# Kernel optimization log

Hardware: AMD Instinct MI355X
Metric: run time of the kernel (lower is better)

The kernel has to match this reference:

```python
import jax, jax.numpy as jnp
import numpy as np

HIDDEN = 768
HEADS = 12
HEAD_DIM = HIDDEN // HEADS


def setup_inputs() -> dict:
    key = jax.random.key(0)
    ks = jax.random.split(key, 9)
    B, S = 2, 2048
    scale = 1.0 / np.sqrt(HIDDEN)
    return {
        "hidden_states": jax.random.normal(ks[0], (B, S, HIDDEN), jnp.float32),
        "context": jax.random.normal(ks[1], (B, S, HIDDEN), jnp.float32),
        "attention_mask": jnp.zeros((B, 1, 1, S), jnp.float32),
        "Wq": jax.random.normal(ks[2], (HIDDEN, HIDDEN), jnp.float32) * scale,
        "bq": jnp.zeros((HIDDEN,), jnp.float32),
        "Wk": jax.random.normal(ks[3], (HIDDEN, HIDDEN), jnp.float32) * scale,
        "bk": jnp.zeros((HIDDEN,), jnp.float32),
        "Wv": jax.random.normal(ks[4], (HIDDEN, HIDDEN), jnp.float32) * scale,
        "bv": jnp.zeros((HIDDEN,), jnp.float32),
    }


def _split_heads(x):
    # [B, S, H*D] -> [B, H, S, D]
    B, S, _ = x.shape
    return x.reshape(B, S, HEADS, HEAD_DIM).transpose(0, 2, 1, 3)


def reference(hidden_states, context, attention_mask, Wq, bq, Wk, bk, Wv, bv):
    # torch Linear: y = x @ W^T + b
    q = _split_heads(hidden_states @ Wq.T + bq)   # [B,H,Sq,D]
    k = _split_heads(context @ Wk.T + bk)         # [B,H,Sk,D]
    v = _split_heads(context @ Wv.T + bv)         # [B,H,Sk,D]

    scores = jnp.einsum("bhqd,bhkd->bhqk", q, k)
    scores = scores / np.sqrt(HEAD_DIM + 1e-05)
    scores = scores + attention_mask
    probs = jax.nn.softmax(scores, axis=-1)       # dropout p=0 -> identity (eval)
    ctx = jnp.einsum("bhqk,bhkd->bhqd", probs, v) # [B,H,Sq,D]
    B, H, Sq, D = ctx.shape
    return ctx.transpose(0, 2, 1, 3).reshape(B, Sq, H * D)
```

## Files before the change

kernel.cpp:

```cpp
#include <hip/hip_runtime.h>
#include <hip/hip_bf16.h>
#include <math.h>

typedef short s16x8 __attribute__((ext_vector_type(8)));
typedef float f32x4 __attribute__((ext_vector_type(4)));
typedef _Float16 f16x4 __attribute__((ext_vector_type(4)));
typedef __fp16 fp16x2 __attribute__((ext_vector_type(2)));
typedef unsigned short u16;

#define NHEADS 12
#define SEQ 2048
#define NBH 24
#define KDIM 768
#define NSPL 4
#define LOG2E 1.44269504088896f

#define SWZ(row, col) (((row) * 64) + ((col) ^ (((row) & 7) << 3)))

#define GLOAD_LDS16(g, l) __builtin_amdgcn_global_load_lds( \
    (const __attribute__((address_space(1))) unsigned int*)(g), \
    (__attribute__((address_space(3))) unsigned int*)(l), 16, 0, 0)

static __device__ __forceinline__ u16 f2bf(float f) {
    union { float f; unsigned u; } v; v.f = f;
    unsigned r = v.u + 0x7fffu + ((v.u >> 16) & 1u);
    return (u16)(r >> 16);
}
static __device__ __forceinline__ u16 f2h(float f) {
    union { _Float16 h; u16 u; } v; v.h = (_Float16)f;
    return v.u;
}
static __device__ __forceinline__ f16x4 pack4(float a, float b, float c, float d) {
    union { fp16x2 h2[2]; f16x4 h4; } u;
    u.h2[0] = __builtin_amdgcn_cvt_pkrtz(a, b);
    u.h2[1] = __builtin_amdgcn_cvt_pkrtz(c, d);
    return u.h4;
}

__global__ void cvt6_kernel(const float* __restrict__ s0, const float* __restrict__ s1,
                            const float* __restrict__ s2, const float* __restrict__ s3,
                            const float* __restrict__ s4, const float* __restrict__ s5,
                            u16* __restrict__ d0, u16* __restrict__ d1, u16* __restrict__ d2,
                            u16* __restrict__ d3, u16* __restrict__ d4, float* __restrict__ d5,
                            int n4a, int n4w, float qscl) {
    const int z = blockIdx.z;
    int i = blockIdx.x * blockDim.x + threadIdx.x;
    if (z == 5) {
        if (i < (2 * SEQ) / 4) {
            float4 f = ((const float4*)s5)[i];
            f.x *= LOG2E; f.y *= LOG2E; f.z *= LOG2E; f.w *= LOG2E;
            ((float4*)d5)[i] = f;
        }
        return;
    }
    const float* src = (z == 0) ? s0 : (z == 1) ? s1 : (z == 2) ? s2 : (z == 3) ? s3 : s4;
    u16* dst         = (z == 0) ? d0 : (z == 1) ? d1 : (z == 2) ? d2 : (z == 3) ? d3 : d4;
    const int n4     = (z < 2) ? n4a : n4w;
    const float scl  = (z == 2) ? qscl : 1.0f;
    if (i < n4) {
        float4 f = ((const float4*)src)[i];
        ushort4 o;
        o.x = f2bf(f.x * scl); o.y = f2bf(f.y * scl); o.z = f2bf(f.z * scl); o.w = f2bf(f.w * scl);
        ((ushort4*)dst)[i] = o;
    }
}

__launch_bounds__(256)
__global__ void qkv_gemm(const u16* __restrict__ X, const u16* __restrict__ C,
                         const u16* __restrict__ W0, const u16* __restrict__ W1, const u16* __restrict__ W2,
                         const float* __restrict__ b0, const float* __restrict__ b1, const float* __restrict__ b2,
                         u16* __restrict__ Qo, u16* __restrict__ Ko, u16* __restrict__ Vo, float qscl) {
    const int z = blockIdx.z;
    const u16* A    = (z == 0) ? X  : C;
    const u16* W    = (z == 0) ? W0 : (z == 1) ? W1 : W2;
    const float* bi = (z == 0) ? b0 : (z == 1) ? b1 : b2;
    u16* out        = (z == 0) ? Qo : (z == 1) ? Ko : Vo;
    const float bscl = (z == 0) ? qscl : 1.0f;

    __shared__ u16 As[3][4096];
    __shared__ u16 Bs[3][4096];

    const int tid  = threadIdx.x;
    const int lane = tid & 63;
    const int wid  = tid >> 6;
    const int wr = wid >> 1, wc = wid & 1;
    const int l15 = lane & 15, lh = lane >> 4;
    const int mBase = blockIdx.x * 128;
    const int nBase = blockIdx.y * 128;

    size_t aSrc[2], bSrc[2]; int ldsOff[2];
    #pragma unroll
    for (int i = 0; i < 2; ++i) {
        int L = i * 2048 + tid * 8;
        int prow = L >> 6;
        int pcol = (L & 63) ^ ((prow & 7) << 3);
        int row = (prow << 1) | (pcol >> 5);
        int col = pcol & 31;
        aSrc[i] = (size_t)(mBase + row) * KDIM + col;
        bSrc[i] = (size_t)(nBase + row) * KDIM + col;
        ldsOff[i] = i * 2048 + wid * 512;
    }

#define G_STAGE(step, buf) do { \
        const size_t kb_ = (size_t)(step) * 32; \
        GLOAD_LDS16(&A[aSrc[0] + kb_], &As[buf][ldsOff[0]]); \
        GLOAD_LDS16(&A[aSrc[1] + kb_], &As[buf][ldsOff[1]]); \
        GLOAD_LDS16(&W[bSrc[0] + kb_], &Bs[buf][ldsOff[0]]); \
        GLOAD_LDS16(&W[bSrc[1] + kb_], &Bs[buf][ldsOff[1]]); \
    } while (0)

    f32x4 acc[4][4] = {};

    G_STAGE(0, 0);
    G_STAGE(1, 1);

    const int NIT = KDIM / 32;
    int cur = 0;
    for (int it = 0; it < NIT; ++it) {
        if (it + 1 < NIT) asm volatile("s_waitcnt vmcnt(4)" ::: "memory");
        else              asm volatile("s_waitcnt vmcnt(0)" ::: "memory");
        __builtin_amdgcn_s_barrier();
        __builtin_amdgcn_sched_barrier(0);

        s16x8 xf[4], wf[4];
        #pragma unroll
        for (int m = 0; m < 4; ++m) {
            int row = wr * 64 + m * 16 + l15;
            xf[m] = *(const s16x8*)(&As[cur][SWZ(row >> 1, (row & 1) * 32 + lh * 8)]);
        }
        #pragma unroll
        for (int n = 0; n < 4; ++n) {
            int row = wc * 64 + n * 16 + l15;
            wf[n] = *(const s16x8*)(&Bs[cur][SWZ(row >> 1, (row & 1) * 32 + lh * 8)]);
        }
        if (z < 2) {
            #pragma unroll
            for (int m = 0; m < 4; ++m)
                #pragma unroll
                for (int n = 0; n < 4; ++n)
                    acc[m][n] = __builtin_amdgcn_mfma_f32_16x16x32_bf16(wf[n], xf[m], acc[m][n], 0, 0, 0);
        } else {
            #pragma unroll
            for (int m = 0; m < 4; ++m)
                #pragma unroll
                for (int n = 0; n < 4; ++n)
                    acc[m][n] = __builtin_amdgcn_mfma_f32_16x16x32_bf16(xf[m], wf[n], acc[m][n], 0, 0, 0);
        }

        if (it + 2 < NIT) {
            int nxt = cur + 2; if (nxt >= 3) nxt -= 3;
            G_STAGE(it + 2, nxt);
        }
        ++cur; if (cur == 3) cur = 0;
    }
#undef G_STAGE

    if (z < 2) {
        #pragma unroll
        for (int m = 0; m < 4; ++m) {
            int sg = mBase + wr * 64 + m * 16 + l15;
            int b = sg >> 11, s = sg & 2047;
            #pragma unroll
            for (int n = 0; n < 4; ++n) {
                int d0 = nBase + wc * 64 + n * 16 + lh * 4;
                int h = d0 >> 6, d = d0 & 63;
                float4 bv = *(const float4*)(&bi[d0]);
                ushort4 o;
                o.x = f2bf(acc[m][n][0] + bv.x * bscl);
                o.y = f2bf(acc[m][n][1] + bv.y * bscl);
                o.z = f2bf(acc[m][n][2] + bv.z * bscl);
                o.w = f2bf(acc[m][n][3] + bv.w * bscl);
                *(ushort4*)(&out[(((size_t)(b * NHEADS + h) * SEQ + s) << 6) + d]) = o;
            }
        }
    } else {
        #pragma unroll
        for (int m = 0; m < 4; ++m) {
            #pragma unroll
            for (int n = 0; n < 4; ++n) {
                int colg = nBase + wc * 64 + n * 16 + l15;
                float bv = bi[colg];
                int h = colg >> 6, d = colg & 63;
                int rowg0 = mBase + wr * 64 + m * 16 + lh * 4;
                int b = rowg0 >> 11, s = rowg0 & 2047;
                int sp = (s & ~0x3C) | (((s >> 2) & 3) << 4) | (((s >> 4) & 3) << 2);
                ushort4 o;
                o.x = f2h(acc[m][n][0] + bv);
                o.y = f2h(acc[m][n][1] + bv);
                o.z = f2h(acc[m][n][2] + bv);
                o.w = f2h(acc[m][n][3] + bv);
                *(ushort4*)(&out[(((size_t)(b * NHEADS + h) * 64 + d) << 11) + sp]) = o;
            }
        }
    }
}

template<int NSPLIT>
__launch_bounds__(512)
__global__ void attn_kernel(const u16* __restrict__ Qg, const u16* __restrict__ Kg,
                            const u16* __restrict__ Vg,
                            const float* __restrict__ maskL, float* __restrict__ out,
                            u16* __restrict__ OpartH, float* __restrict__ MLpart) {
    constexpr int NT = SEQ / 64 / NSPLIT;
    __shared__ u16 Ks[2][64 * 64];
    __shared__ u16 Vt[2][64 * 64];
    __shared__ float maskLds[NT * 64];

    const int tid  = threadIdx.x;
    const int lane = tid & 63;
    const int wid  = tid >> 6;

    int qx, bh, z;
    if (NSPLIT == 4) {
        int L = blockIdx.x + 16 * (blockIdx.y + NBH * blockIdx.z);
        int xcd = L & 7, idx = L >> 3;
        int grp = xcd * 12 + (idx >> 4);
        qx = idx & 15;
        bh = grp % NBH;
        z  = grp / NBH;
    } else {
        qx = blockIdx.x; bh = blockIdx.y; z = 0;
    }
    const int b = bh / NHEADS;
    const int h = bh % NHEADS;
    const int q0 = qx * 128 + wid * 16;
    const int l15 = lane & 15, lh = lane >> 4;
    const int tile0 = z * NT;

    for (int i = tid * 4; i < NT * 64; i += 512 * 4)
        *(float4*)(&maskLds[i]) = *(const float4*)(&maskL[(size_t)b * SEQ + (tile0 << 6) + i]);

    const int srow = tid >> 3;
    const int scol = ((tid & 7) * 8) ^ ((srow & 7) << 3);
    const size_t kSrc = (((size_t)bh * SEQ + srow) << 6) + scol + ((size_t)tile0 << 12);
    const size_t vSrc = (((size_t)bh * 64 + srow) << 11) + scol + (size_t)tile0 * 64;
    const int ldsBase = wid * 512;

    s16x8 qf[2];
    #pragma unroll
    for (int kk = 0; kk < 2; ++kk)
        qf[kk] = *(const s16x8*)(&Qg[(((size_t)bh * SEQ + q0 + l15) << 6) + kk * 32 + lh * 8]);

    f32x4 oacc[4] = {};
    float mrun = -1e30f, lrun = 0.f;

    GLOAD_LDS16(&Kg[kSrc], &Ks[0][ldsBase]);
    GLOAD_LDS16(&Vg[vSrc], &Vt[0][ldsBase]);

    for (int t = 0; t < NT; ++t) {
        const int cur = t & 1;
        __syncthreads();
        if (t + 1 < NT) {
            GLOAD_LDS16(&Kg[kSrc + ((size_t)(t + 1) << 12)], &Ks[cur ^ 1][ldsBase]);
            GLOAD_LDS16(&Vg[vSrc + (size_t)(t + 1) * 64],    &Vt[cur ^ 1][ldsBase]);
        }

        f32x4 sacc[4];
        #pragma unroll
        for (int n = 0; n < 4; ++n) {
            float4 mv = *(const float4*)(&maskLds[t * 64 + n * 16 + lh * 4]);
            sacc[n][0] = mv.x; sacc[n][1] = mv.y; sacc[n][2] = mv.z; sacc[n][3] = mv.w;
        }
        __builtin_amdgcn_s_setprio(1);
        #pragma unroll
        for (int kk = 0; kk < 2; ++kk) {
            #pragma unroll
            for (int n = 0; n < 4; ++n) {
                s16x8 kf = *(const s16x8*)(&Ks[cur][SWZ(n * 16 + l15, kk * 32 + lh * 8)]);
                sacc[n] = __builtin_amdgcn_mfma_f32_16x16x32_bf16(kf, qf[kk], sacc[n], 0, 0, 0);
            }
        }
        __builtin_amdgcn_s_setprio(0);

        float tmax = sacc[0][0];
        #pragma unroll
        for (int n = 0; n < 4; ++n)
            #pragma unroll
            for (int j = 0; j < 4; ++j)
                tmax = fmaxf(tmax, sacc[n][j]);

        if (!__all(tmax - mrun <= 11.0f)) {
            float rmax = fmaxf(tmax, __shfl_xor(tmax, 16));
            rmax = fmaxf(rmax, __shfl_xor(rmax, 32));
            float mnew = fmaxf(mrun, rmax);
            float alpha = __builtin_amdgcn_exp2f(mrun - mnew);
            lrun *= alpha;
            #pragma unroll
            for (int nd = 0; nd < 4; ++nd)
                #pragma unroll
                for (int j = 0; j < 4; ++j)
                    oacc[nd][j] *= alpha;
            mrun = mnew;
        }

        f16x4 pf[4];
        #pragma unroll
        for (int n = 0; n < 4; ++n) {
            float p0 = __builtin_amdgcn_exp2f(sacc[n][0] - mrun);
            float p1 = __builtin_amdgcn_exp2f(sacc[n][1] - mrun);
            float p2 = __builtin_amdgcn_exp2f(sacc[n][2] - mrun);
            float p3 = __builtin_amdgcn_exp2f(sacc[n][3] - mrun);
            lrun += (p0 + p1) + (p2 + p3);
            pf[n] = pack4(p0, p1, p2, p3);
        }

        __builtin_amdgcn_s_setprio(1);
        #pragma unroll
        for (int kk = 0; kk < 2; ++kk) {
            #pragma unroll
            for (int nd = 0; nd < 4; ++nd) {
                s16x8 v2 = *(const s16x8*)(&Vt[cur][SWZ(nd * 16 + l15, lh * 16 + kk * 8)]);
                union { s16x8 s8; f16x4 h4[2]; } u; u.s8 = v2;
                oacc[nd] = __builtin_amdgcn_mfma_f32_16x16x16f16(u.h4[0], pf[2 * kk],     oacc[nd], 0, 0, 0);
                oacc[nd] = __builtin_amdgcn_mfma_f32_16x16x16f16(u.h4[1], pf[2 * kk + 1], oacc[nd], 0, 0, 0);
            }
        }
        __builtin_amdgcn_s_setprio(0);
    }

    lrun += __shfl_xor(lrun, 16);
    lrun += __shfl_xor(lrun, 32);

    const float inv = 1.0f / lrun;
    const int s = q0 + l15;
    if (NSPLIT == 1) {
        #pragma unroll
        for (int nd = 0; nd < 4; ++nd) {
            float4 o;
            o.x = oacc[nd][0] * inv; o.y = oacc[nd][1] * inv;
            o.z = oacc[nd][2] * inv; o.w = oacc[nd][3] * inv;
            *(float4*)(&out[(size_t)(b * SEQ + s) * (NHEADS * 64) + h * 64 + nd * 16 + lh * 4]) = o;
        }
    } else {
        const size_t rbase = ((size_t)(z * NBH + bh) * SEQ + s);
        #pragma unroll
        for (int nd = 0; nd < 4; ++nd) {
            union { f16x4 h4; ushort4 u4; } o;
            o.h4 = pack4(oacc[nd][0] * inv, oacc[nd][1] * inv,
                         oacc[nd][2] * inv, oacc[nd][3] * inv);
            *(ushort4*)(&OpartH[rbase * 64 + nd * 16 + lh * 4]) = o.u4;
        }
        if (lh == 0)
            *(float2*)(&MLpart[rbase * 2]) = make_float2(mrun, lrun);
    }
}

__global__ void combine_kernel(const u16* __restrict__ OpartH, const float* __restrict__ MLpart,
                               float* __restrict__ out) {
    int gid = blockIdx.x * 256 + threadIdx.x;
    int row = gid >> 4, d4 = gid & 15;
    float2 ml[NSPL];
    float m = -1e30f;
    #pragma unroll
    for (int k = 0; k < NSPL; ++k) {
        ml[k] = ((const float2*)MLpart)[(size_t)k * NBH * SEQ + row];
        m = fmaxf(m, ml[k].x);
    }
    float w[NSPL], wsum = 0.f;
    #pragma unroll
    for (int k = 0; k < NSPL; ++k) {
        w[k] = __builtin_amdgcn_exp2f(ml[k].x - m) * ml[k].y;
        wsum += w[k];
    }
    float inv = 1.0f / wsum;
    float4 o = {0.f, 0.f, 0.f, 0.f};
    #pragma unroll
    for (int k = 0; k < NSPL; ++k) {
        union { ushort4 u4; f16x4 h4; } a;
        a.u4 = *(const ushort4*)(&OpartH[((size_t)k * NBH * SEQ + row) * 64 + d4 * 4]);
        float wk = w[k] * inv;
        o.x += (float)a.h4[0] * wk; o.y += (float)a.h4[1] * wk;
        o.z += (float)a.h4[2] * wk; o.w += (float)a.h4[3] * wk;
    }
    int bh = row >> 11, s = row & 2047;
    int b = bh / NHEADS, hh = bh % NHEADS;
    *(float4*)(&out[(size_t)(b * SEQ + s) * (NHEADS * 64) + hh * 64 + d4 * 4]) = o;
}

extern "C" void kernel_launch(void* const* d_in, const int* in_sizes, int n_in,
                              void* d_out, int out_size, void* d_ws, size_t ws_size,
                              hipStream_t stream) {
    const float* hidden  = (const float*)d_in[0];
    const float* context = (const float*)d_in[1];
    const float* mask    = (const float*)d_in[2];
    const float* Wq = (const float*)d_in[3];
    const float* bq = (const float*)d_in[4];
    const float* Wk = (const float*)d_in[5];
    const float* bk = (const float*)d_in[6];
    const float* Wv = (const float*)d_in[7];
    const float* bv = (const float*)d_in[8];
    float* out = (float*)d_out;

    char* ws = (char*)d_ws;
    const size_t XSZ = (size_t)4096 * 768 * 2;
    const size_t WSZ = (size_t)768 * 768 * 2;
    u16* X16  = (u16*)(ws);
    u16* C16  = (u16*)(ws + XSZ);
    u16* W16q = (u16*)(ws + 2 * XSZ);
    u16* W16k = (u16*)(ws + 2 * XSZ + WSZ);
    u16* W16v = (u16*)(ws + 2 * XSZ + 2 * WSZ);
    u16* Q16  = (u16*)(ws + 2 * XSZ + 3 * WSZ);
    u16* K16  = (u16*)(ws + 3 * XSZ + 3 * WSZ);
    u16* V16  = (u16*)(ws + 4 * XSZ + 3 * WSZ);
    const size_t MASKL_OFF = 5 * XSZ + 3 * WSZ;
    float* maskL = (float*)(ws + MASKL_OFF);
    const size_t OPART_OFF = MASKL_OFF + 2 * SEQ * sizeof(float) + 256;
    u16* OpartH = (u16*)(ws + OPART_OFF);
    const size_t ML_OFF = OPART_OFF + (size_t)NSPL * NBH * SEQ * 64 * 2;
    float* MLpart = (float*)(ws + ML_OFF);
    const size_t WS_NEED_SPLIT = ML_OFF + (size_t)NSPL * NBH * SEQ * 2 * 4;

    const float qscl = (float)((1.0 / sqrt(64.0 + 1e-5)) * 1.44269504088896);

    const int n4x = 4096 * 768 / 4;
    const int n4w = 768 * 768 / 4;
    cvt6_kernel<<<dim3((n4x + 255) / 256, 1, 6), 256, 0, stream>>>(
        hidden, context, Wq, Wk, Wv, mask,
        X16, C16, W16q, W16k, W16v, maskL, n4x, n4w, qscl);

    qkv_gemm<<<dim3(4096 / 128, 768 / 128, 3), 256, 0, stream>>>(
        X16, C16, W16q, W16k, W16v, bq, bk, bv, Q16, K16, V16, qscl);

    if (ws_size >= WS_NEED_SPLIT) {
        attn_kernel<NSPL><<<dim3(SEQ / 128, NBH, NSPL), 512, 0, stream>>>(
            Q16, K16, V16, maskL, out, OpartH, MLpart);
        combine_kernel<<<(NBH * SEQ * 16) / 256, 256, 0, stream>>>(OpartH, MLpart, out);
    } else {
        attn_kernel<1><<<dim3(SEQ / 128, NBH, 1), 512, 0, stream>>>(
            Q16, K16, V16, maskL, out, OpartH, MLpart);
    }
}
```

Measured before the change: 97.05 us.

## Process two query groups per wave with 256-thread blocks and two-way KV split

Each wave now handles 32 query rows as two 16-row groups, so every K and V fragment read from shared memory feeds two MFMAs. Blocks shrink to 4 waves that each issue two async loads per tile, and the KV split drops from four to two, with the XCD-aware block mapping adjusted to match. The aim is to cut LDS traffic per MFMA and reduce the partial-output combine work, at the cost of more registers per wave, fewer resident waves, and a longer serial KV loop per block.

```diff
diff --git a/kernel.cpp b/kernel.cpp
--- a/kernel.cpp
+++ b/kernel.cpp
@@ -12,7 +12,7 @@
 #define SEQ 2048
 #define NBH 24
 #define KDIM 768
-#define NSPL 4
+#define NSPL 2
 #define LOG2E 1.44269504088896f
 
 #define SWZ(row, col) (((row) * 64) + ((col) ^ (((row) & 7) << 3)))
@@ -196,14 +196,14 @@
 }
 
 template<int NSPLIT>
-__launch_bounds__(512)
+__launch_bounds__(256)
 __global__ void attn_kernel(const u16* __restrict__ Qg, const u16* __restrict__ Kg,
                             const u16* __restrict__ Vg,
                             const float* __restrict__ maskL, float* __restrict__ out,
                             u16* __restrict__ OpartH, float* __restrict__ MLpart) {
     constexpr int NT = SEQ / 64 / NSPLIT;
-    __shared__ u16 Ks[2][64 * 64];
-    __shared__ u16 Vt[2][64 * 64];
+    __shared__ u16 Ks[2][4096];
+    __shared__ u16 Vt[2][4096];
     __shared__ float maskLds[NT * 64];
 
     const int tid  = threadIdx.x;
@@ -211,10 +211,10 @@
     const int wid  = tid >> 6;
 
     int qx, bh, z;
-    if (NSPLIT == 4) {
+    if (NSPLIT == 2) {
         int L = blockIdx.x + 16 * (blockIdx.y + NBH * blockIdx.z);
         int xcd = L & 7, idx = L >> 3;
-        int grp = xcd * 12 + (idx >> 4);
+        int grp = xcd * 6 + (idx >> 4);
         qx = idx & 15;
         bh = grp % NBH;
         z  = grp / NBH;
@@ -223,43 +223,59 @@
     }
     const int b = bh / NHEADS;
     const int h = bh % NHEADS;
-    const int q0 = qx * 128 + wid * 16;
+    const int q0 = qx * 128 + wid * 32;
     const int l15 = lane & 15, lh = lane >> 4;
     const int tile0 = z * NT;
 
-    for (int i = tid * 4; i < NT * 64; i += 512 * 4)
+    for (int i = tid * 4; i < NT * 64; i += 256 * 4)
         *(float4*)(&maskLds[i]) = *(const float4*)(&maskL[(size_t)b * SEQ + (tile0 << 6) + i]);
 
-    const int srow = tid >> 3;
-    const int scol = ((tid & 7) * 8) ^ ((srow & 7) << 3);
-    const size_t kSrc = (((size_t)bh * SEQ + srow) << 6) + scol + ((size_t)tile0 << 12);
-    const size_t vSrc = (((size_t)bh * 64 + srow) << 11) + scol + (size_t)tile0 * 64;
-    const int ldsBase = wid * 512;
-
-    s16x8 qf[2];
-    #pragma unroll
-    for (int kk = 0; kk < 2; ++kk)
-        qf[kk] = *(const s16x8*)(&Qg[(((size_t)bh * SEQ + q0 + l15) << 6) + kk * 32 + lh * 8]);
-
-    f32x4 oacc[4] = {};
-    float mrun = -1e30f, lrun = 0.f;
-
-    GLOAD_LDS16(&Kg[kSrc], &Ks[0][ldsBase]);
-    GLOAD_LDS16(&Vg[vSrc], &Vt[0][ldsBase]);
+    int srow[2], scol[2]; size_t kSrc[2], vSrc[2]; int ldsOff[2];
+    #pragma unroll
+    for (int i = 0; i < 2; ++i) {
+        srow[i] = i * 32 + (tid >> 3);
+        scol[i] = ((tid & 7) * 8) ^ ((srow[i] & 7) << 3);
+        kSrc[i] = (((size_t)bh * SEQ + srow[i]) << 6) + scol[i] + ((size_t)tile0 << 12);
+        vSrc[i] = (((size_t)bh * 64 + srow[i]) << 11) + scol[i] + (size_t)tile0 * 64;
+        ldsOff[i] = i * 2048 + wid * 512;
+    }
+
+    s16x8 qf[2][2];
+    #pragma unroll
+    for (int g = 0; g < 2; ++g)
+        #pragma unroll
+        for (int kk = 0; kk < 2; ++kk)
+            qf[g][kk] = *(const s16x8*)(&Qg[(((size_t)bh * SEQ + q0 + g * 16 + l15) << 6) + kk * 32 + lh * 8]);
+
+    f32x4 oacc[2][4] = {};
+    float mrun[2] = {-1e30f, -1e30f}, lrun[2] = {0.f, 0.f};
+
+    #pragma unroll
+    for (int i = 0; i < 2; ++i) {
+        GLOAD_LDS16(&Kg[kSrc[i]], &Ks[0][ldsOff[i]]);
+        GLOAD_LDS16(&Vg[vSrc[i]], &Vt[0][ldsOff[i]]);
+    }
 
     for (int t = 0; t < NT; ++t) {
         const int cur = t & 1;
         __syncthreads();
         if (t + 1 < NT) {
-            GLOAD_LDS16(&Kg[kSrc + ((size_t)(t + 1) << 12)], &Ks[cur ^ 1][ldsBase]);
-            GLOAD_LDS16(&Vg[vSrc + (size_t)(t + 1) * 64],    &Vt[cur ^ 1][ldsBase]);
-        }
-
-        f32x4 sacc[4];
+            #pragma unroll
+            for (int i = 0; i < 2; ++i) {
+                GLOAD_LDS16(&Kg[kSrc[i] + ((size_t)(t + 1) << 12)], &Ks[cur ^ 1][ldsOff[i]]);
+                GLOAD_LDS16(&Vg[vSrc[i] + (size_t)(t + 1) * 64],    &Vt[cur ^ 1][ldsOff[i]]);
+            }
+        }
+
+        f32x4 sacc[2][4];
         #pragma unroll
         for (int n = 0; n < 4; ++n) {
             float4 mv = *(const float4*)(&maskLds[t * 64 + n * 16 + lh * 4]);
-            sacc[n][0] = mv.x; sacc[n][1] = mv.y; sacc[n][2] = mv.z; sacc[n][3] = mv.w;
+            #pragma unroll
+            for (int g = 0; g < 2; ++g) {
+                sacc[g][n][0] = mv.x; sacc[g][n][1] = mv.y;
+                sacc[g][n][2] = mv.z; sacc[g][n][3] = mv.w;
+            }
         }
         __builtin_amdgcn_s_setprio(1);
         #pragma unroll
@@ -267,42 +283,52 @@
             #pragma unroll
             for (int n = 0; n < 4; ++n) {
                 s16x8 kf = *(const s16x8*)(&Ks[cur][SWZ(n * 16 + l15, kk * 32 + lh * 8)]);
-                sacc[n] = __builtin_amdgcn_mfma_f32_16x16x32_bf16(kf, qf[kk], sacc[n], 0, 0, 0);
+                sacc[0][n] = __builtin_amdgcn_mfma_f32_16x16x32_bf16(kf, qf[0][kk], sacc[0][n], 0, 0, 0);
+                sacc[1][n] = __builtin_amdgcn_mfma_f32_16x16x32_bf16(kf, qf[1][kk], sacc[1][n], 0, 0, 0);
             }
         }
         __builtin_amdgcn_s_setprio(0);
 
-        float tmax = sacc[0][0];
+        float tmax0 = sacc[0][0][0], tmax1 = sacc[1][0][0];
         #pragma unroll
         for (int n = 0; n < 4; ++n)
             #pragma unroll
-            for (int j = 0; j < 4; ++j)
-                tmax = fmaxf(tmax, sacc[n][j]);
-
-        if (!__all(tmax - mrun <= 11.0f)) {
-            float rmax = fmaxf(tmax, __shfl_xor(tmax, 16));
-            rmax = fmaxf(rmax, __shfl_xor(rmax, 32));
-            float mnew = fmaxf(mrun, rmax);
-            float alpha = __builtin_amdgcn_exp2f(mrun - mnew);
-            lrun *= alpha;
+            for (int j = 0; j < 4; ++j) {
+                tmax0 = fmaxf(tmax0, sacc[0][n][j]);
+                tmax1 = fmaxf(tmax1, sacc[1][n][j]);
+            }
+
+        if (!__all(fmaxf(tmax0 - mrun[0], tmax1 - mrun[1]) <= 11.0f)) {
+            float r0 = fmaxf(tmax0, __shfl_xor(tmax0, 16));
+            r0 = fmaxf(r0, __shfl_xor(r0, 32));
+            float r1 = fmaxf(tmax1, __shfl_xor(tmax1, 16));
+            r1 = fmaxf(r1, __shfl_xor(r1, 32));
+            float mn0 = fmaxf(mrun[0], r0), mn1 = fmaxf(mrun[1], r1);
+            float a0 = __builtin_amdgcn_exp2f(mrun[0] - mn0);
+            float a1 = __builtin_amdgcn_exp2f(mrun[1] - mn1);
+            lrun[0] *= a0; lrun[1] *= a1;
             #pragma unroll
             for (int nd = 0; nd < 4; ++nd)
                 #pragma unroll
-                for (int j = 0; j < 4; ++j)
-                    oacc[nd][j] *= alpha;
-            mrun = mnew;
-        }
-
-        f16x4 pf[4];
-        #pragma unroll
-        for (int n = 0; n < 4; ++n) {
-            float p0 = __builtin_amdgcn_exp2f(sacc[n][0] - mrun);
-            float p1 = __builtin_amdgcn_exp2f(sacc[n][1] - mrun);
-            float p2 = __builtin_amdgcn_exp2f(sacc[n][2] - mrun);
-            float p3 = __builtin_amdgcn_exp2f(sacc[n][3] - mrun);
-            lrun += (p0 + p1) + (p2 + p3);
-            pf[n] = pack4(p0, p1, p2, p3);
-        }
+                for (int j = 0; j < 4; ++j) {
+                    oacc[0][nd][j] *= a0;
+                    oacc[1][nd][j] *= a1;
+                }
+            mrun[0] = mn0; mrun[1] = mn1;
+        }
+
+        f16x4 pf[2][4];
+        #pragma unroll
+        for (int g = 0; g < 2; ++g)
+            #pragma unroll
+            for (int n = 0; n < 4; ++n) {
+                float p0 = __builtin_amdgcn_exp2f(sacc[g][n][0] - mrun[g]);
+                float p1 = __builtin_amdgcn_exp2f(sacc[g][n][1] - mrun[g]);
+                float p2 = __builtin_amdgcn_exp2f(sacc[g][n][2] - mrun[g]);
+                float p3 = __builtin_amdgcn_exp2f(sacc[g][n][3] - mrun[g]);
+                lrun[g] += (p0 + p1) + (p2 + p3);
+                pf[g][n] = pack4(p0, p1, p2, p3);
+            }
 
         __builtin_amdgcn_s_setprio(1);
         #pragma unroll
@@ -311,37 +337,41 @@
             for (int nd = 0; nd < 4; ++nd) {
                 s16x8 v2 = *(const s16x8*)(&Vt[cur][SWZ(nd * 16 + l15, lh * 16 + kk * 8)]);
                 union { s16x8 s8; f16x4 h4[2]; } u; u.s8 = v2;
-                oacc[nd] = __builtin_amdgcn_mfma_f32_16x16x16f16(u.h4[0], pf[2 * kk],     oacc[nd], 0, 0, 0);
-                oacc[nd] = __builtin_amdgcn_mfma_f32_16x16x16f16(u.h4[1], pf[2 * kk + 1], oacc[nd], 0, 0, 0);
+                oacc[0][nd] = __builtin_amdgcn_mfma_f32_16x16x16f16(u.h4[0], pf[0][2 * kk],     oacc[0][nd], 0, 0, 0);
+                oacc[0][nd] = __builtin_amdgcn_mfma_f32_16x16x16f16(u.h4[1], pf[0][2 * kk + 1], oacc[0][nd], 0, 0, 0);
+                oacc[1][nd] = __builtin_amdgcn_mfma_f32_16x16x16f16(u.h4[0], pf[1][2 * kk],     oacc[1][nd], 0, 0, 0);
+                oacc[1][nd] = __builtin_amdgcn_mfma_f32_16x16x16f16(u.h4[1], pf[1][2 * kk + 1], oacc[1][nd], 0, 0, 0);
             }
         }
         __builtin_amdgcn_s_setprio(0);
     }
 
-    lrun += __shfl_xor(lrun, 16);
-    lrun += __shfl_xor(lrun, 32);
-
-    const float inv = 1.0f / lrun;
-    const int s = q0 + l15;
-    if (NSPLIT == 1) {
-        #pragma unroll
-        for (int nd = 0; nd < 4; ++nd) {
-            float4 o;
-            o.x = oacc[nd][0] * inv; o.y = oacc[nd][1] * inv;
-            o.z = oacc[nd][2] * inv; o.w = oacc[nd][3] * inv;
-            *(float4*)(&out[(size_t)(b * SEQ + s) * (NHEADS * 64) + h * 64 + nd * 16 + lh * 4]) = o;
-        }
-    } else {
-        const size_t rbase = ((size_t)(z * NBH + bh) * SEQ + s);
-        #pragma unroll
-        for (int nd = 0; nd < 4; ++nd) {
-            union { f16x4 h4; ushort4 u4; } o;
-            o.h4 = pack4(oacc[nd][0] * inv, oacc[nd][1] * inv,
-                         oacc[nd][2] * inv, oacc[nd][3] * inv);
-            *(ushort4*)(&OpartH[rbase * 64 + nd * 16 + lh * 4]) = o.u4;
-        }
-        if (lh == 0)
-            *(float2*)(&MLpart[rbase * 2]) = make_float2(mrun, lrun);
+    #pragma unroll
+    for (int g = 0; g < 2; ++g) {
+        lrun[g] += __shfl_xor(lrun[g], 16);
+        lrun[g] += __shfl_xor(lrun[g], 32);
+        const float inv = 1.0f / lrun[g];
+        const int s = q0 + g * 16 + l15;
+        if (NSPLIT == 1) {
+            #pragma unroll
+            for (int nd = 0; nd < 4; ++nd) {
+                float4 o;
+                o.x = oacc[g][nd][0] * inv; o.y = oacc[g][nd][1] * inv;
+                o.z = oacc[g][nd][2] * inv; o.w = oacc[g][nd][3] * inv;
+                *(float4*)(&out[(size_t)(b * SEQ + s) * (NHEADS * 64) + h * 64 + nd * 16 + lh * 4]) = o;
+            }
+        } else {
+            const size_t rbase = ((size_t)(z * NBH + bh) * SEQ + s);
+            #pragma unroll
+            for (int nd = 0; nd < 4; ++nd) {
+                union { f16x4 h4; ushort4 u4; } o;
+                o.h4 = pack4(oacc[g][nd][0] * inv, oacc[g][nd][1] * inv,
+                             oacc[g][nd][2] * inv, oacc[g][nd][3] * inv);
+                *(ushort4*)(&OpartH[rbase * 64 + nd * 16 + lh * 4]) = o.u4;
+            }
+            if (lh == 0)
+                *(float2*)(&MLpart[rbase * 2]) = make_float2(mrun[g], lrun[g]);
+        }
     }
 }
 
@@ -422,11 +452,11 @@
         X16, C16, W16q, W16k, W16v, bq, bk, bv, Q16, K16, V16, qscl);
 
     if (ws_size >= WS_NEED_SPLIT) {
-        attn_kernel<NSPL><<<dim3(SEQ / 128, NBH, NSPL), 512, 0, stream>>>(
+        attn_kernel<NSPL><<<dim3(SEQ / 128, NBH, NSPL), 256, 0, stream>>>(
             Q16, K16, V16, maskL, out, OpartH, MLpart);
         combine_kernel<<<(NBH * SEQ * 16) / 256, 256, 0, stream>>>(OpartH, MLpart, out);
     } else {
-        attn_kernel<1><<<dim3(SEQ / 128, NBH, 1), 512, 0, stream>>>(
+        attn_kernel<1><<<dim3(SEQ / 128, NBH, 1), 256, 0, stream>>>(
             Q16, K16, V16, maskL, out, OpartH, MLpart);
     }
 }
```

After: 103.6 us. 1.07x slower.
